# Kernel optimization log

Measured on AMD Instinct MI355X. Metric: run time of the kernel, lower is better.

Reference implementation:

```python
import jax, jax.numpy as jnp
import numpy as np
from jax import lax

DILATION_DEPTH = 10
N_REPEAT = 5
DILS = [2 ** i for i in range(DILATION_DEPTH)] * N_REPEAT  # 50 layers
N_RES, N_SKIP, N_FEAT = 32, 512, 8
B, T = 4, 16384


def _dconv(x, w, b, d):
    # valid (causal, no padding) dilated conv1d, kernel size 2: out[t] = w0*x[t] + w1*x[t+d]
    y = lax.conv_general_dilated(x, w, window_strides=(1,), padding='VALID',
                                 rhs_dilation=(d,), dimension_numbers=('NCH', 'OIH', 'NCH'))
    return y + b[None, :, None]


def _pw(x, w, b):
    # 1x1 conv as einsum; w: [out, in]
    return jnp.einsum('oc,bct->bot', w, x) + b[None, :, None]


def setup_inputs() -> dict:
    key = jax.random.key(0)
    ks = jax.random.split(key, 16)
    L = len(DILS)
    s = 0.1
    return {
        'input': jax.random.normal(ks[0], (B, T, N_FEAT), dtype=jnp.float32),
        'from_w': jax.random.normal(ks[1], (N_RES, N_FEAT, 1), dtype=jnp.float32) * s,
        'from_b': jax.random.normal(ks[2], (N_RES,), dtype=jnp.float32) * s,
        'sig_w': jax.random.normal(ks[3], (L, N_RES, N_RES, 2), dtype=jnp.float32) * s,
        'sig_b': jax.random.normal(ks[4], (L, N_RES), dtype=jnp.float32) * s,
        'tan_w': jax.random.normal(ks[5], (L, N_RES, N_RES, 2), dtype=jnp.float32) * s,
        'tan_b': jax.random.normal(ks[6], (L, N_RES), dtype=jnp.float32) * s,
        'skip_w': jax.random.normal(ks[7], (L, N_SKIP, N_RES, 1), dtype=jnp.float32) * s,
        'skip_b': jax.random.normal(ks[8], (L, N_SKIP), dtype=jnp.float32) * s,
        'res_w': jax.random.normal(ks[9], (L, N_RES, N_RES, 1), dtype=jnp.float32) * s,
        'res_b': jax.random.normal(ks[10], (L, N_RES), dtype=jnp.float32) * s,
        'post1_w': jax.random.normal(ks[11], (N_SKIP, N_SKIP, 1), dtype=jnp.float32) * s,
        'post1_b': jax.random.normal(ks[12], (N_SKIP,), dtype=jnp.float32) * s,
        'post2_w': jax.random.normal(ks[13], (1, N_SKIP, 1), dtype=jnp.float32) * s,
        'post2_b': jax.random.normal(ks[14], (1,), dtype=jnp.float32) * s,
    }


def reference(input, from_w, from_b, sig_w, sig_b, tan_w, tan_b,
              skip_w, skip_b, res_w, res_b, post1_w, post1_b, post2_w, post2_b):
    h = jnp.transpose(input, (0, 2, 1))                       # [B, F, T]
    h = _pw(h, from_w[:, :, 0], from_b)                       # [B, 32, T]
    Lout = h.shape[2] - sum(DILS)                             # final output length
    skip_sum = jnp.zeros((h.shape[0], N_SKIP, Lout), dtype=h.dtype)
    for i, d in enumerate(DILS):
        gate = jax.nn.sigmoid(_dconv(h, sig_w[i], sig_b[i], d)) * \
               jnp.tanh(_dconv(h, tan_w[i], tan_b[i], d))      # [B, 32, T_i - d]
        skip = _pw(gate, skip_w[i, :, :, 0], skip_b[i])        # [B, 512, T_i - d]
        skip_sum = skip_sum + skip[:, :, -Lout:]
        h = _pw(gate, res_w[i, :, :, 0], res_b[i]) + h[:, :, d:]
    o = jax.nn.elu(skip_sum)
    o = _pw(o, post1_w[:, :, 0], post1_b)
    o = jax.nn.elu(o)
    o = _pw(o, post2_w[:, :, 0], post2_b)                     # [B, 1, Lout]
    return o
```

## Files before the change

### kernel.cpp

```cpp
#include <hip/hip_runtime.h>
#include <hip/hip_bf16.h>

#define TLEN 16384
#define NB 4
#define NLAYER 50
#define SUMD 5115
#define LOUT 11269
#define K1 (NLAYER * 32)
#define MSKIP 512
#define FWOUT 256
#define FWIN 511
#define FP 36

typedef unsigned short u16;
typedef __attribute__((ext_vector_type(4))) float f32x4;
typedef __attribute__((ext_vector_type(8))) __bf16 bf16x8;

__device__ __forceinline__ u16 f2bf(float f) {
  __hip_bfloat16 h = __float2bfloat16(f);
  return *reinterpret_cast<u16*>(&h);
}
__device__ __forceinline__ float bf2f(u16 u) {
  __hip_bfloat16 h = *reinterpret_cast<__hip_bfloat16*>(&u);
  return __bfloat162float(h);
}

__global__ __launch_bounds__(256) void prep_k(
    const float* __restrict__ skip_w, const float* __restrict__ skip_b,
    const float* __restrict__ post1_w,
    const float* __restrict__ sig_w, const float* __restrict__ tan_w,
    const float* __restrict__ res_w,
    u16* __restrict__ Wskip, u16* __restrict__ P1, float* __restrict__ biasS,
    u16* __restrict__ WC, u16* __restrict__ RC) {
  int t = blockIdx.x * 256 + threadIdx.x;
  const int n1 = 512 * K1;
  const int n2 = n1 + 512 * 512;
  const int n3 = n2 + 512;
  const int n4 = n3 + NLAYER * 64 * 64;
  const int n5 = n4 + NLAYER * 32 * 32;
  if (t < n1) {
    int m = t / K1, k = t - m * K1;
    int i = k >> 5, c = k & 31;
    Wskip[t] = f2bf(skip_w[((size_t)i * 512 + m) * 32 + c]);
  } else if (t < n2) {
    int z = t - n1;
    P1[z] = f2bf(post1_w[z]);
  } else if (t < n3) {
    int c = t - n2;
    float s = 0.f;
    for (int i = 0; i < NLAYER; i++) s += skip_b[i * 512 + c];
    biasS[c] = s;
  } else if (t < n4) {
    int z = t - n3;
    int l = z >> 12, rem = z & 4095, o = rem >> 6, k = rem & 63;
    int c = k & 31, lr = k >> 5;
    float v;
    if (o < 32) v = sig_w[(((size_t)l * 32 + o) * 32 + c) * 2 + lr];
    else        v = tan_w[(((size_t)l * 32 + (o - 32)) * 32 + c) * 2 + lr];
    WC[z] = f2bf(v);
  } else if (t < n5) {
    int z = t - n4;
    int l = z >> 10, rem = z & 1023, o = rem >> 5, c = rem & 31;
    RC[z] = f2bf(res_w[((size_t)l * 32 + o) * 32 + c]);
  }
}

__global__ __launch_bounds__(256) void init_p(
    const float* __restrict__ inp, const float* __restrict__ fw,
    const float* __restrict__ fb, float* __restrict__ H, int t0, int cw) {
  __shared__ float FWs[256];
  __shared__ float FBs[32];
  int tid = threadIdx.x;
  FWs[tid] = fw[tid];
  if (tid < 32) FBs[tid] = fb[tid];
  __syncthreads();
  int gsz = gridDim.x * 256;
  int gid0 = blockIdx.x * 256 + tid;
  for (int b = 0; b < NB; b++) {
    const float* ib = inp + ((size_t)b * TLEN + t0) * 8;
    float* hb = H + (size_t)b * cw * 32;
    for (int p = gid0; p < cw; p += gsz) {
      float4 x0 = *reinterpret_cast<const float4*>(ib + (size_t)p * 8);
      float4 x1 = *reinterpret_cast<const float4*>(ib + (size_t)p * 8 + 4);
      float x[8] = {x0.x, x0.y, x0.z, x0.w, x1.x, x1.y, x1.z, x1.w};
      float* op = hb + (size_t)p * 32;
      #pragma unroll
      for (int r4 = 0; r4 < 8; r4++) {
        float4 o;
        #pragma unroll
        for (int j = 0; j < 4; j++) {
          int r = r4 * 4 + j;
          float acc = FBs[r];
          #pragma unroll
          for (int f = 0; f < 8; f++) acc += FWs[r * 8 + f] * x[f];
          ((float*)&o)[j] = acc;
        }
        *reinterpret_cast<float4*>(op + r4 * 4) = o;
      }
    }
  }
}

__global__ __launch_bounds__(512, 1) void fuse8_k(
    const float* __restrict__ src, float* __restrict__ dst,
    u16* __restrict__ G,
    const u16* __restrict__ WC, const u16* __restrict__ RC,
    const float* __restrict__ sb, const float* __restrict__ tb,
    const float* __restrict__ rb,
    int L0, int len_in, int cw, int clen) {
  __shared__ float HB[2][FWIN][FP];
  __shared__ u16 GT[8][16][40];
  int tid = threadIdx.x;
  int wv = tid >> 6, lane = tid & 63;
  int pc = lane & 15, kg = lane >> 4;
  int b = blockIdx.y;
  int len_out = len_in - 255;
  int pstart = cw - len_out + blockIdx.x * FWOUT;
  int g0 = pstart - 255;
  int wcount = (cw - g0 < FWIN) ? (cw - g0) : FWIN;
  int ocount = (cw - pstart < FWOUT) ? (cw - pstart) : FWOUT;

  const float* sp = src + ((size_t)b * cw + g0) * 32;
  for (int z = tid; z < wcount * 8; z += 512) {
    int lp = z >> 3, c4 = z & 7;
    *reinterpret_cast<float4*>(&HB[0][lp][c4 * 4]) =
        *reinterpret_cast<const float4*>(sp + (size_t)lp * 32 + c4 * 4);
  }
  __syncthreads();

  int cur = 0;
  for (int l = 0; l < 8; l++) {
    int d = 1 << l;
    int cumD = (2 << l) - 1;
    const u16* Wc = WC + (size_t)(L0 + l) * 4096;
    const u16* Rc = RC + (size_t)(L0 + l) * 1024;
    bf16x8 AW[4][2], AR[2];
    #pragma unroll
    for (int mt = 0; mt < 4; mt++) {
      AW[mt][0] = *reinterpret_cast<const bf16x8*>(Wc + (mt * 16 + pc) * 64 + kg * 8);
      AW[mt][1] = *reinterpret_cast<const bf16x8*>(Wc + (mt * 16 + pc) * 64 + 32 + kg * 8);
    }
    AR[0] = *reinterpret_cast<const bf16x8*>(Rc + pc * 32 + kg * 8);
    AR[1] = *reinterpret_cast<const bf16x8*>(Rc + (16 + pc) * 32 + kg * 8);
    float4 sbv0 = *reinterpret_cast<const float4*>(sb + (L0 + l) * 32 + kg * 4);
    float4 sbv1 = *reinterpret_cast<const float4*>(sb + (L0 + l) * 32 + 16 + kg * 4);
    float4 tbv0 = *reinterpret_cast<const float4*>(tb + (L0 + l) * 32 + kg * 4);
    float4 tbv1 = *reinterpret_cast<const float4*>(tb + (L0 + l) * 32 + 16 + kg * 4);
    float4 rbv0 = *reinterpret_cast<const float4*>(rb + (L0 + l) * 32 + kg * 4);
    float4 rbv1 = *reinterpret_cast<const float4*>(rb + (L0 + l) * 32 + 16 + kg * 4);

    int lo_local = wcount - cumD;
    int nit = (lo_local + 127) >> 7;
    for (int t = 0; t < nit; t++) {
      int lp = cumD + t * 128 + wv * 16 + pc;
      bool valid = lp < wcount;
      int lpc = valid ? lp : wcount - 1;

      float4 r0 = *reinterpret_cast<const float4*>(&HB[cur][lpc][kg * 8]);
      float4 r1 = *reinterpret_cast<const float4*>(&HB[cur][lpc][kg * 8 + 4]);
      float4 l0v = *reinterpret_cast<const float4*>(&HB[cur][lpc - d][kg * 8]);
      float4 l1v = *reinterpret_cast<const float4*>(&HB[cur][lpc - d][kg * 8 + 4]);

      union { u16 u[8]; bf16x8 v; } uL, uR;
      {
        float lf[8] = {l0v.x, l0v.y, l0v.z, l0v.w, l1v.x, l1v.y, l1v.z, l1v.w};
        float rf[8] = {r0.x, r0.y, r0.z, r0.w, r1.x, r1.y, r1.z, r1.w};
        #pragma unroll
        for (int j = 0; j < 8; j++) { uL.u[j] = f2bf(lf[j]); uR.u[j] = f2bf(rf[j]); }
      }

      f32x4 cs0 = {0.f, 0.f, 0.f, 0.f}, cs1 = {0.f, 0.f, 0.f, 0.f};
      f32x4 ct0 = {0.f, 0.f, 0.f, 0.f}, ct1 = {0.f, 0.f, 0.f, 0.f};
      cs0 = __builtin_amdgcn_mfma_f32_16x16x32_bf16(AW[0][0], uL.v, cs0, 0, 0, 0);
      cs0 = __builtin_amdgcn_mfma_f32_16x16x32_bf16(AW[0][1], uR.v, cs0, 0, 0, 0);
      cs1 = __builtin_amdgcn_mfma_f32_16x16x32_bf16(AW[1][0], uL.v, cs1, 0, 0, 0);
      cs1 = __builtin_amdgcn_mfma_f32_16x16x32_bf16(AW[1][1], uR.v, cs1, 0, 0, 0);
      ct0 = __builtin_amdgcn_mfma_f32_16x16x32_bf16(AW[2][0], uL.v, ct0, 0, 0, 0);
      ct0 = __builtin_amdgcn_mfma_f32_16x16x32_bf16(AW[2][1], uR.v, ct0, 0, 0, 0);
      ct1 = __builtin_amdgcn_mfma_f32_16x16x32_bf16(AW[3][0], uL.v, ct1, 0, 0, 0);
      ct1 = __builtin_amdgcn_mfma_f32_16x16x32_bf16(AW[3][1], uR.v, ct1, 0, 0, 0);

      u16 gs0[4], gs1[4];
      {
        float sa[4] = {sbv0.x, sbv0.y, sbv0.z, sbv0.w};
        float sbq[4] = {sbv1.x, sbv1.y, sbv1.z, sbv1.w};
        float ta[4] = {tbv0.x, tbv0.y, tbv0.z, tbv0.w};
        float tbq[4] = {tbv1.x, tbv1.y, tbv1.z, tbv1.w};
        #pragma unroll
        for (int r = 0; r < 4; r++) {
          float s0 = cs0[r] + sa[r], t0v = ct0[r] + ta[r];
          float s1 = cs1[r] + sbq[r], t1v = ct1[r] + tbq[r];
          float g0v = (1.f / (1.f + __expf(-s0))) * (2.f / (1.f + __expf(-2.f * t0v)) - 1.f);
          float g1v = (1.f / (1.f + __expf(-s1))) * (2.f / (1.f + __expf(-2.f * t1v)) - 1.f);
          gs0[r] = f2bf(g0v);
          gs1[r] = f2bf(g1v);
        }
      }
      uint2 pk0 = {(unsigned)gs0[0] | ((unsigned)gs0[1] << 16),
                   (unsigned)gs0[2] | ((unsigned)gs0[3] << 16)};
      uint2 pk1 = {(unsigned)gs1[0] | ((unsigned)gs1[1] << 16),
                   (unsigned)gs1[2] | ((unsigned)gs1[3] << 16)};
      *reinterpret_cast<uint2*>(&GT[wv][pc][kg * 4]) = pk0;
      *reinterpret_cast<uint2*>(&GT[wv][pc][16 + kg * 4]) = pk1;

      int p = g0 + lpc;
      if (valid && p >= pstart && p < pstart + ocount && p >= cw - clen) {
        int n = b * clen + (p - (cw - clen));
        u16* gr = G + (size_t)n * K1 + (L0 + l) * 32;
        *reinterpret_cast<uint2*>(gr + kg * 4) = pk0;
        *reinterpret_cast<uint2*>(gr + 16 + kg * 4) = pk1;
      }

      bf16x8 bg = *reinterpret_cast<const bf16x8*>(&GT[wv][pc][kg * 8]);
      float4 ha = *reinterpret_cast<const float4*>(&HB[cur][lpc][kg * 4]);
      float4 hb2 = *reinterpret_cast<const float4*>(&HB[cur][lpc][16 + kg * 4]);
      f32x4 h0 = {ha.x + rbv0.x, ha.y + rbv0.y, ha.z + rbv0.z, ha.w + rbv0.w};
      f32x4 h1 = {hb2.x + rbv1.x, hb2.y + rbv1.y, hb2.z + rbv1.z, hb2.w + rbv1.w};
      f32x4 d0 = __builtin_amdgcn_mfma_f32_16x16x32_bf16(AR[0], bg, h0, 0, 0, 0);
      f32x4 d1 = __builtin_amdgcn_mfma_f32_16x16x32_bf16(AR[1], bg, h1, 0, 0, 0);
      if (valid) {
        *reinterpret_cast<float4*>(&HB[cur ^ 1][lp][kg * 4]) = float4{d0[0], d0[1], d0[2], d0[3]};
        *reinterpret_cast<float4*>(&HB[cur ^ 1][lp][16 + kg * 4]) = float4{d1[0], d1[1], d1[2], d1[3]};
      }
    }
    __syncthreads();
    cur ^= 1;
  }

  float* dp = dst + ((size_t)b * cw + pstart) * 32;
  for (int z = tid; z < ocount * 8; z += 512) {
    int lp = z >> 3, c4 = z & 7;
    *reinterpret_cast<float4*>(dp + (size_t)lp * 32 + c4 * 4) =
        *reinterpret_cast<float4*>(&HB[cur][255 + lp][c4 * 4]);
  }
}

__global__ __launch_bounds__(256, 2) void layer_p(
    const float* __restrict__ src, float* __restrict__ dst,
    u16* __restrict__ G,
    const u16* __restrict__ Wc, const u16* __restrict__ Rc,
    const float* __restrict__ sbl, const float* __restrict__ tbl,
    const float* __restrict__ rbl,
    int layer, int d, int lo, int cw, int clen) {
  __shared__ u16 GT[4][16][40];
  __shared__ float HRT[4][16][36];
  int tid = threadIdx.x;
  int wv = tid >> 6, lane = tid & 63;
  int pc = lane & 15, kg = lane >> 4;
  int b = blockIdx.y;

  bf16x8 AW[4][2], AR[2];
  #pragma unroll
  for (int mt = 0; mt < 4; mt++) {
    AW[mt][0] = *reinterpret_cast<const bf16x8*>(Wc + (mt * 16 + pc) * 64 + kg * 8);
    AW[mt][1] = *reinterpret_cast<const bf16x8*>(Wc + (mt * 16 + pc) * 64 + 32 + kg * 8);
  }
  AR[0] = *reinterpret_cast<const bf16x8*>(Rc + pc * 32 + kg * 8);
  AR[1] = *reinterpret_cast<const bf16x8*>(Rc + (16 + pc) * 32 + kg * 8);

  float4 sbv0 = *reinterpret_cast<const float4*>(sbl + kg * 4);
  float4 sbv1 = *reinterpret_cast<const float4*>(sbl + 16 + kg * 4);
  float4 tbv0 = *reinterpret_cast<const float4*>(tbl + kg * 4);
  float4 tbv1 = *reinterpret_cast<const float4*>(tbl + 16 + kg * 4);
  float4 rbv0 = *reinterpret_cast<const float4*>(rbl + kg * 4);
  float4 rbv1 = *reinterpret_cast<const float4*>(rbl + 16 + kg * 4);

  int idx = blockIdx.x * 64 + wv * 16 + pc;
  bool valid = idx < lo;
  int idc = valid ? idx : lo - 1;
  int p = cw - lo + idc;

  const float* hp = src + ((size_t)b * cw + p) * 32 + kg * 8;
  float4 r0 = *reinterpret_cast<const float4*>(hp);
  float4 r1 = *reinterpret_cast<const float4*>(hp + 4);
  const float* hq = hp - (size_t)d * 32;
  float4 l0 = *reinterpret_cast<const float4*>(hq);
  float4 l1 = *reinterpret_cast<const float4*>(hq + 4);

  union { u16 u[8]; bf16x8 v; } uL, uR;
  {
    float lf[8] = {l0.x, l0.y, l0.z, l0.w, l1.x, l1.y, l1.z, l1.w};
    float rf[8] = {r0.x, r0.y, r0.z, r0.w, r1.x, r1.y, r1.z, r1.w};
    #pragma unroll
    for (int j = 0; j < 8; j++) { uL.u[j] = f2bf(lf[j]); uR.u[j] = f2bf(rf[j]); }
  }
  *reinterpret_cast<float4*>(&HRT[wv][pc][kg * 8]) = r0;
  *reinterpret_cast<float4*>(&HRT[wv][pc][kg * 8 + 4]) = r1;

  f32x4 cs0 = {0.f, 0.f, 0.f, 0.f}, cs1 = {0.f, 0.f, 0.f, 0.f};
  f32x4 ct0 = {0.f, 0.f, 0.f, 0.f}, ct1 = {0.f, 0.f, 0.f, 0.f};
  cs0 = __builtin_amdgcn_mfma_f32_16x16x32_bf16(AW[0][0], uL.v, cs0, 0, 0, 0);
  cs0 = __builtin_amdgcn_mfma_f32_16x16x32_bf16(AW[0][1], uR.v, cs0, 0, 0, 0);
  cs1 = __builtin_amdgcn_mfma_f32_16x16x32_bf16(AW[1][0], uL.v, cs1, 0, 0, 0);
  cs1 = __builtin_amdgcn_mfma_f32_16x16x32_bf16(AW[1][1], uR.v, cs1, 0, 0, 0);
  ct0 = __builtin_amdgcn_mfma_f32_16x16x32_bf16(AW[2][0], uL.v, ct0, 0, 0, 0);
  ct0 = __builtin_amdgcn_mfma_f32_16x16x32_bf16(AW[2][1], uR.v, ct0, 0, 0, 0);
  ct1 = __builtin_amdgcn_mfma_f32_16x16x32_bf16(AW[3][0], uL.v, ct1, 0, 0, 0);
  ct1 = __builtin_amdgcn_mfma_f32_16x16x32_bf16(AW[3][1], uR.v, ct1, 0, 0, 0);

  u16 gs0[4], gs1[4];
  {
    float sa[4] = {sbv0.x, sbv0.y, sbv0.z, sbv0.w};
    float sbq[4] = {sbv1.x, sbv1.y, sbv1.z, sbv1.w};
    float ta[4] = {tbv0.x, tbv0.y, tbv0.z, tbv0.w};
    float tbq[4] = {tbv1.x, tbv1.y, tbv1.z, tbv1.w};
    #pragma unroll
    for (int r = 0; r < 4; r++) {
      float s0 = cs0[r] + sa[r], t0v = ct0[r] + ta[r];
      float s1 = cs1[r] + sbq[r], t1v = ct1[r] + tbq[r];
      float g0 = (1.f / (1.f + __expf(-s0))) * (2.f / (1.f + __expf(-2.f * t0v)) - 1.f);
      float g1 = (1.f / (1.f + __expf(-s1))) * (2.f / (1.f + __expf(-2.f * t1v)) - 1.f);
      gs0[r] = f2bf(g0);
      gs1[r] = f2bf(g1);
    }
  }
  uint2 pk0 = {(unsigned)gs0[0] | ((unsigned)gs0[1] << 16),
               (unsigned)gs0[2] | ((unsigned)gs0[3] << 16)};
  uint2 pk1 = {(unsigned)gs1[0] | ((unsigned)gs1[1] << 16),
               (unsigned)gs1[2] | ((unsigned)gs1[3] << 16)};
  *reinterpret_cast<uint2*>(&GT[wv][pc][kg * 4]) = pk0;
  *reinterpret_cast<uint2*>(&GT[wv][pc][16 + kg * 4]) = pk1;

  if (valid && p >= cw - clen) {
    int n = b * clen + (p - (cw - clen));
    u16* gr = G + (size_t)n * K1 + layer * 32;
    *reinterpret_cast<uint2*>(gr + kg * 4) = pk0;
    *reinterpret_cast<uint2*>(gr + 16 + kg * 4) = pk1;
  }

  bf16x8 bg = *reinterpret_cast<const bf16x8*>(&GT[wv][pc][kg * 8]);
  float4 ha = *reinterpret_cast<const float4*>(&HRT[wv][pc][kg * 4]);
  float4 hbq = *reinterpret_cast<const float4*>(&HRT[wv][pc][16 + kg * 4]);
  f32x4 h0 = {ha.x + rbv0.x, ha.y + rbv0.y, ha.z + rbv0.z, ha.w + rbv0.w};
  f32x4 h1 = {hbq.x + rbv1.x, hbq.y + rbv1.y, hbq.z + rbv1.z, hbq.w + rbv1.w};
  f32x4 d0 = __builtin_amdgcn_mfma_f32_16x16x32_bf16(AR[0], bg, h0, 0, 0, 0);
  f32x4 d1 = __builtin_amdgcn_mfma_f32_16x16x32_bf16(AR[1], bg, h1, 0, 0, 0);
  if (valid) {
    float* dp = dst + ((size_t)b * cw + p) * 32;
    *reinterpret_cast<float4*>(dp + kg * 4) = float4{d0[0], d0[1], d0[2], d0[3]};
    *reinterpret_cast<float4*>(dp + 16 + kg * 4) = float4{d1[0], d1[1], d1[2], d1[3]};
  }
}

__global__ __launch_bounds__(256) void gemm_k(
    const u16* __restrict__ A, const u16* __restrict__ B,
    const float* __restrict__ bias, u16* __restrict__ Out,
    int N, int K) {
  __shared__ u16 As[128][72];
  __shared__ u16 Bs[128][72];
  int tid = threadIdx.x;

  int nwg = gridDim.x;
  int orig = blockIdx.x;
  int q = nwg >> 3, r8 = nwg & 7, xcd = orig & 7, sl = orig >> 3;
  int wg = (xcd < r8 ? xcd * (q + 1) : r8 * (q + 1) + (xcd - r8) * q) + sl;
  int m0 = (wg & 3) * 128;
  int n0 = (wg >> 2) * 128;

  int lane = tid & 63, w = tid >> 6;
  int wm = w >> 1, wn = w & 1;

  f32x4 acc[4][4];
  #pragma unroll
  for (int i = 0; i < 4; i++)
    #pragma unroll
    for (int j = 0; j < 4; j++) acc[i][j] = f32x4{0.f, 0.f, 0.f, 0.f};

  int rS = tid >> 1, qS = tid & 1;
  for (int k0 = 0; k0 < K; k0 += 64) {
    {
      const uint4* asrc = reinterpret_cast<const uint4*>(A + (size_t)(m0 + rS) * K + k0 + qS * 32);
      uint4 a0 = asrc[0], a1 = asrc[1], a2 = asrc[2], a3 = asrc[3];
      *reinterpret_cast<uint4*>(&As[rS][qS * 32]) = a0;
      *reinterpret_cast<uint4*>(&As[rS][qS * 32 + 8]) = a1;
      *reinterpret_cast<uint4*>(&As[rS][qS * 32 + 16]) = a2;
      *reinterpret_cast<uint4*>(&As[rS][qS * 32 + 24]) = a3;
    }
    {
      int nr = n0 + rS;
      uint4 b0 = {0,0,0,0}, b1 = {0,0,0,0}, b2 = {0,0,0,0}, b3 = {0,0,0,0};
      if (nr < N) {
        const uint4* bsrc = reinterpret_cast<const uint4*>(B + (size_t)nr * K + k0 + qS * 32);
        b0 = bsrc[0]; b1 = bsrc[1]; b2 = bsrc[2]; b3 = bsrc[3];
      }
      *reinterpret_cast<uint4*>(&Bs[rS][qS * 32]) = b0;
      *reinterpret_cast<uint4*>(&Bs[rS][qS * 32 + 8]) = b1;
      *reinterpret_cast<uint4*>(&Bs[rS][qS * 32 + 16]) = b2;
      *reinterpret_cast<uint4*>(&Bs[rS][qS * 32 + 24]) = b3;
    }
    __syncthreads();

    int row16 = lane & 15, kg = lane >> 4;
    #pragma unroll
    for (int s = 0; s < 2; s++) {
      bf16x8 af[4], bfr[4];
      #pragma unroll
      for (int mf = 0; mf < 4; mf++)
        af[mf] = *reinterpret_cast<const bf16x8*>(&As[wm * 64 + mf * 16 + row16][s * 32 + kg * 8]);
      #pragma unroll
      for (int nf = 0; nf < 4; nf++)
        bfr[nf] = *reinterpret_cast<const bf16x8*>(&Bs[wn * 64 + nf * 16 + row16][s * 32 + kg * 8]);
      #pragma unroll
      for (int mf = 0; mf < 4; mf++)
        #pragma unroll
        for (int nf = 0; nf < 4; nf++)
          acc[mf][nf] = __builtin_amdgcn_mfma_f32_16x16x32_bf16(af[mf], bfr[nf], acc[mf][nf], 0, 0, 0);
    }
    __syncthreads();
  }

  #pragma unroll
  for (int mf = 0; mf < 4; mf++) {
    int rowb = m0 + wm * 64 + mf * 16 + (lane >> 4) * 4;
    float b0 = bias[rowb], b1 = bias[rowb + 1], b2 = bias[rowb + 2], b3 = bias[rowb + 3];
    #pragma unroll
    for (int nf = 0; nf < 4; nf++) {
      int col = n0 + wn * 64 + nf * 16 + (lane & 15);
      if (col < N) {
        float v0 = acc[mf][nf][0] + b0, v1 = acc[mf][nf][1] + b1;
        float v2 = acc[mf][nf][2] + b2, v3 = acc[mf][nf][3] + b3;
        v0 = v0 > 0.f ? v0 : expm1f(v0);
        v1 = v1 > 0.f ? v1 : expm1f(v1);
        v2 = v2 > 0.f ? v2 : expm1f(v2);
        v3 = v3 > 0.f ? v3 : expm1f(v3);
        uint2 pk = {(unsigned)f2bf(v0) | ((unsigned)f2bf(v1) << 16),
                    (unsigned)f2bf(v2) | ((unsigned)f2bf(v3) << 16)};
        *reinterpret_cast<uint2*>(Out + (size_t)col * 512 + rowb) = pk;
      }
    }
  }
}

__global__ __launch_bounds__(256) void final_k(
    const u16* __restrict__ E2, const float* __restrict__ w,
    const float* __restrict__ bptr, float* __restrict__ out,
    int Nc, int clen, int t0) {
  int gid = blockIdx.x * 256 + threadIdx.x;
  int n = gid >> 2, qq = gid & 3;
  if (n >= Nc) return;
  const uint4* row = reinterpret_cast<const uint4*>(E2 + (size_t)n * 512 + qq * 128);
  const float4* wq = reinterpret_cast<const float4*>(w + qq * 128);
  float acc = 0.f;
  #pragma unroll 4
  for (int c8 = 0; c8 < 16; c8++) {
    uint4 v = row[c8];
    float4 w0 = wq[c8 * 2], w1 = wq[c8 * 2 + 1];
    acc += w0.x * bf2f(v.x & 0xffff) + w0.y * bf2f(v.x >> 16)
         + w0.z * bf2f(v.y & 0xffff) + w0.w * bf2f(v.y >> 16)
         + w1.x * bf2f(v.z & 0xffff) + w1.y * bf2f(v.z >> 16)
         + w1.z * bf2f(v.w & 0xffff) + w1.w * bf2f(v.w >> 16);
  }
  acc += __shfl_xor(acc, 1);
  acc += __shfl_xor(acc, 2);
  if (qq == 0) {
    int b = n / clen, tc = n - b * clen;
    out[(size_t)b * LOUT + t0 + tc] = acc + bptr[0];
  }
}

extern "C" void kernel_launch(void* const* d_in, const int* in_sizes, int n_in,
                              void* d_out, int out_size, void* d_ws, size_t ws_size,
                              hipStream_t stream) {
  const float* input   = (const float*)d_in[0];
  const float* from_w  = (const float*)d_in[1];
  const float* from_b  = (const float*)d_in[2];
  const float* sig_w   = (const float*)d_in[3];
  const float* sig_b   = (const float*)d_in[4];
  const float* tan_w   = (const float*)d_in[5];
  const float* tan_b   = (const float*)d_in[6];
  const float* skip_w  = (const float*)d_in[7];
  const float* skip_b  = (const float*)d_in[8];
  const float* res_w   = (const float*)d_in[9];
  const float* res_b   = (const float*)d_in[10];
  const float* post1_w = (const float*)d_in[11];
  const float* post1_b = (const float*)d_in[12];
  const float* post2_w = (const float*)d_in[13];
  const float* post2_b = (const float*)d_in[14];

  auto al = [](size_t x) { return (x + 255) & ~(size_t)255; };
  size_t oW  = 0;
  size_t oP1 = oW  + al((size_t)512 * K1 * 2);
  size_t oB  = oP1 + al((size_t)512 * 512 * 2);
  size_t oWC = oB  + al((size_t)512 * 4);
  size_t oRC = oWC + al((size_t)NLAYER * 64 * 64 * 2);
  size_t wend = oRC + al((size_t)NLAYER * 32 * 32 * 2);

  int NC = 32, CL = 0;
  size_t oH0 = wend, oH1 = wend, oG = wend, oE = wend;
  const int cand[6] = {1, 2, 4, 8, 16, 32};
  for (int ci = 0; ci < 6; ci++) {
    int nc = cand[ci];
    int cl = (LOUT + nc - 1) / nc;
    int cw = cl + SUMD;
    size_t hB = al((size_t)NB * 32 * cw * 4);
    size_t gB = al((size_t)NB * cl * K1 * 2);
    size_t eB = al((size_t)512 * NB * cl * 2);
    size_t need = wend + 2 * hB + gB + eB;
    if (need <= ws_size || nc == 32) {
      NC = nc; CL = cl;
      oH0 = wend; oH1 = oH0 + hB; oG = oH1 + hB; oE = oG + gB;
      break;
    }
  }

  char* ws = (char*)d_ws;
  u16*   Wskip = (u16*)(ws + oW);
  u16*   P1    = (u16*)(ws + oP1);
  float* biasS = (float*)(ws + oB);
  u16*   WC    = (u16*)(ws + oWC);
  u16*   RC    = (u16*)(ws + oRC);
  float* H0    = (float*)(ws + oH0);
  float* H1    = (float*)(ws + oH1);
  u16*   G     = (u16*)(ws + oG);
  u16*   E     = (u16*)(ws + oE);
  u16*   E2    = (u16*)(ws + oG);

  int prep_items = 512 * K1 + 512 * 512 + 512 + NLAYER * 64 * 64 + NLAYER * 32 * 32;
  prep_k<<<(prep_items + 255) / 256, 256, 0, stream>>>(
      skip_w, skip_b, post1_w, sig_w, tan_w, res_w, Wskip, P1, biasS, WC, RC);

  for (int c = 0; c < NC; c++) {
    int t0 = c * CL;
    if (t0 >= LOUT) break;
    int clen = LOUT - t0 < CL ? LOUT - t0 : CL;
    int cw = clen + SUMD;

    init_p<<<256, 256, 0, stream>>>(input, from_w, from_b, H0, t0, cw);

    float* a = H0;
    float* b2 = H1;
    int len = cw;
    for (int cyc = 0; cyc < 5; cyc++) {
      int L0 = cyc * 10;
      int lo8 = len - 255;
      int tiles = (lo8 + FWOUT - 1) / FWOUT;
      fuse8_k<<<dim3(tiles, NB), 512, 0, stream>>>(
          a, b2, G, WC, RC, sig_b, tan_b, res_b, L0, len, cw, clen);
      { float* t = a; a = b2; b2 = t; }
      len = lo8;
      {
        int li = L0 + 8, d = 256;
        int lo = len - d;
        layer_p<<<dim3((lo + 63) / 64, NB), 256, 0, stream>>>(
            a, b2, G, WC + (size_t)li * 4096, RC + (size_t)li * 1024,
            sig_b + li * 32, tan_b + li * 32, res_b + li * 32,
            li, d, lo, cw, clen);
        { float* t = a; a = b2; b2 = t; }
        len = lo;
      }
      {
        int li = L0 + 9, d = 512;
        int lo = len - d;
        layer_p<<<dim3((lo + 63) / 64, NB), 256, 0, stream>>>(
            a, b2, G, WC + (size_t)li * 4096, RC + (size_t)li * 1024,
            sig_b + li * 32, tan_b + li * 32, res_b + li * 32,
            li, d, lo, cw, clen);
        { float* t = a; a = b2; b2 = t; }
        len = lo;
      }
    }

    int Nc = NB * clen;
    int ntile = (Nc + 127) / 128;
    gemm_k<<<4 * ntile, 256, 0, stream>>>(Wskip, G, biasS, E, Nc, K1);
    gemm_k<<<4 * ntile, 256, 0, stream>>>(P1, E, post1_b, E2, Nc, 512);

    final_k<<<(4 * Nc + 255) / 256, 256, 0, stream>>>(E2, post2_w, post2_b, (float*)d_out, Nc, clen, t0);
  }
}
```

Measured before the change: 709.7 us.

## Fuse final projection into post1 GEMM epilogue and use direct global-to-LDS loads

The final 512-to-1 projection is folded into the post1 GEMM epilogue. Each tile reduces its partial dot products across lanes and atomically adds them into the output, which is zeroed beforehand with a memset. This removes the E2 intermediate write and read and one kernel launch per chunk. The GEMM main loop also switches to global_load_lds direct loads with K-step 32 and unpadded LDS, which can add LDS bank conflicts and more barrier iterations; the atomics make the summation order nondeterministic.

```diff
diff --git a/kernel.cpp b/kernel.cpp
--- a/kernel.cpp
+++ b/kernel.cpp
@@ -345,9 +345,11 @@
 __global__ __launch_bounds__(256) void gemm_k(
     const u16* __restrict__ A, const u16* __restrict__ B,
     const float* __restrict__ bias, u16* __restrict__ Out,
-    int N, int K) {
-  __shared__ u16 As[128][72];
-  __shared__ u16 Bs[128][72];
+    const float* __restrict__ w2, const float* __restrict__ b2p,
+    float* __restrict__ outv,
+    int N, int K, int FIN, int clen, int t0f) {
+  __shared__ __align__(16) u16 As[128 * 32];
+  __shared__ __align__(16) u16 Bs[128 * 32];
   int tid = threadIdx.x;
 
   int nwg = gridDim.x;
@@ -357,8 +359,10 @@
   int m0 = (wg & 3) * 128;
   int n0 = (wg >> 2) * 128;
 
-  int lane = tid & 63, w = tid >> 6;
-  int wm = w >> 1, wn = w & 1;
+  int lane = tid & 63, wv = tid >> 6;
+  int wm = wv >> 1, wn = wv & 1;
+  int row16 = lane & 15, kg = lane >> 4;
+  int l3 = lane & 3, lr = lane >> 2;
 
   f32x4 acc[4][4];
   #pragma unroll
@@ -366,95 +370,92 @@
     #pragma unroll
     for (int j = 0; j < 4; j++) acc[i][j] = f32x4{0.f, 0.f, 0.f, 0.f};
 
-  int rS = tid >> 1, qS = tid & 1;
-  for (int k0 = 0; k0 < K; k0 += 64) {
-    {
-      const uint4* asrc = reinterpret_cast<const uint4*>(A + (size_t)(m0 + rS) * K + k0 + qS * 32);
-      uint4 a0 = asrc[0], a1 = asrc[1], a2 = asrc[2], a3 = asrc[3];
-      *reinterpret_cast<uint4*>(&As[rS][qS * 32]) = a0;
-      *reinterpret_cast<uint4*>(&As[rS][qS * 32 + 8]) = a1;
-      *reinterpret_cast<uint4*>(&As[rS][qS * 32 + 16]) = a2;
-      *reinterpret_cast<uint4*>(&As[rS][qS * 32 + 24]) = a3;
-    }
-    {
-      int nr = n0 + rS;
-      uint4 b0 = {0,0,0,0}, b1 = {0,0,0,0}, b2 = {0,0,0,0}, b3 = {0,0,0,0};
-      if (nr < N) {
-        const uint4* bsrc = reinterpret_cast<const uint4*>(B + (size_t)nr * K + k0 + qS * 32);
-        b0 = bsrc[0]; b1 = bsrc[1]; b2 = bsrc[2]; b3 = bsrc[3];
-      }
-      *reinterpret_cast<uint4*>(&Bs[rS][qS * 32]) = b0;
-      *reinterpret_cast<uint4*>(&Bs[rS][qS * 32 + 8]) = b1;
-      *reinterpret_cast<uint4*>(&Bs[rS][qS * 32 + 16]) = b2;
-      *reinterpret_cast<uint4*>(&Bs[rS][qS * 32 + 24]) = b3;
+  for (int k0 = 0; k0 < K; k0 += 32) {
+    #pragma unroll
+    for (int i = 0; i < 2; i++) {
+      int c = wv * 2 + i;
+      int row = c * 16 + lr;
+      const u16* ga = A + (size_t)(m0 + row) * K + k0 + l3 * 8;
+      __builtin_amdgcn_global_load_lds(
+          (const __attribute__((address_space(1))) void*)ga,
+          (__attribute__((address_space(3))) void*)(As + c * 512), 16, 0, 0);
+      int nr = n0 + row;
+      if (nr > N - 1) nr = N - 1;
+      const u16* gb = B + (size_t)nr * K + k0 + l3 * 8;
+      __builtin_amdgcn_global_load_lds(
+          (const __attribute__((address_space(1))) void*)gb,
+          (__attribute__((address_space(3))) void*)(Bs + c * 512), 16, 0, 0);
     }
     __syncthreads();
 
-    int row16 = lane & 15, kg = lane >> 4;
-    #pragma unroll
-    for (int s = 0; s < 2; s++) {
-      bf16x8 af[4], bfr[4];
-      #pragma unroll
-      for (int mf = 0; mf < 4; mf++)
-        af[mf] = *reinterpret_cast<const bf16x8*>(&As[wm * 64 + mf * 16 + row16][s * 32 + kg * 8]);
+    bf16x8 af[4], bfr[4];
+    #pragma unroll
+    for (int mf = 0; mf < 4; mf++)
+      af[mf] = *reinterpret_cast<const bf16x8*>(&As[(wm * 64 + mf * 16 + row16) * 32 + kg * 8]);
+    #pragma unroll
+    for (int nf = 0; nf < 4; nf++)
+      bfr[nf] = *reinterpret_cast<const bf16x8*>(&Bs[(wn * 64 + nf * 16 + row16) * 32 + kg * 8]);
+    #pragma unroll
+    for (int mf = 0; mf < 4; mf++)
       #pragma unroll
       for (int nf = 0; nf < 4; nf++)
-        bfr[nf] = *reinterpret_cast<const bf16x8*>(&Bs[wn * 64 + nf * 16 + row16][s * 32 + kg * 8]);
+        acc[mf][nf] = __builtin_amdgcn_mfma_f32_16x16x32_bf16(af[mf], bfr[nf], acc[mf][nf], 0, 0, 0);
+    __syncthreads();
+  }
+
+  if (!FIN) {
+    #pragma unroll
+    for (int mf = 0; mf < 4; mf++) {
+      int rowb = m0 + wm * 64 + mf * 16 + kg * 4;
+      float b0 = bias[rowb], b1 = bias[rowb + 1], b2 = bias[rowb + 2], b3 = bias[rowb + 3];
       #pragma unroll
-      for (int mf = 0; mf < 4; mf++)
-        #pragma unroll
-        for (int nf = 0; nf < 4; nf++)
-          acc[mf][nf] = __builtin_amdgcn_mfma_f32_16x16x32_bf16(af[mf], bfr[nf], acc[mf][nf], 0, 0, 0);
-    }
-    __syncthreads();
-  }
-
-  #pragma unroll
-  for (int mf = 0; mf < 4; mf++) {
-    int rowb = m0 + wm * 64 + mf * 16 + (lane >> 4) * 4;
-    float b0 = bias[rowb], b1 = bias[rowb + 1], b2 = bias[rowb + 2], b3 = bias[rowb + 3];
-    #pragma unroll
-    for (int nf = 0; nf < 4; nf++) {
-      int col = n0 + wn * 64 + nf * 16 + (lane & 15);
-      if (col < N) {
+      for (int nf = 0; nf < 4; nf++) {
+        int col = n0 + wn * 64 + nf * 16 + row16;
+        if (col < N) {
+          float v0 = acc[mf][nf][0] + b0, v1 = acc[mf][nf][1] + b1;
+          float v2 = acc[mf][nf][2] + b2, v3 = acc[mf][nf][3] + b3;
+          v0 = v0 > 0.f ? v0 : expm1f(v0);
+          v1 = v1 > 0.f ? v1 : expm1f(v1);
+          v2 = v2 > 0.f ? v2 : expm1f(v2);
+          v3 = v3 > 0.f ? v3 : expm1f(v3);
+          uint2 pk = {(unsigned)f2bf(v0) | ((unsigned)f2bf(v1) << 16),
+                      (unsigned)f2bf(v2) | ((unsigned)f2bf(v3) << 16)};
+          *reinterpret_cast<uint2*>(Out + (size_t)col * 512 + rowb) = pk;
+        }
+      }
+    }
+  } else {
+    float part[4] = {0.f, 0.f, 0.f, 0.f};
+    #pragma unroll
+    for (int mf = 0; mf < 4; mf++) {
+      int rowb = m0 + wm * 64 + mf * 16 + kg * 4;
+      float b0 = bias[rowb], b1 = bias[rowb + 1], b2 = bias[rowb + 2], b3 = bias[rowb + 3];
+      float w0 = w2[rowb], w1 = w2[rowb + 1], w2v = w2[rowb + 2], w3 = w2[rowb + 3];
+      #pragma unroll
+      for (int nf = 0; nf < 4; nf++) {
         float v0 = acc[mf][nf][0] + b0, v1 = acc[mf][nf][1] + b1;
         float v2 = acc[mf][nf][2] + b2, v3 = acc[mf][nf][3] + b3;
         v0 = v0 > 0.f ? v0 : expm1f(v0);
         v1 = v1 > 0.f ? v1 : expm1f(v1);
         v2 = v2 > 0.f ? v2 : expm1f(v2);
         v3 = v3 > 0.f ? v3 : expm1f(v3);
-        uint2 pk = {(unsigned)f2bf(v0) | ((unsigned)f2bf(v1) << 16),
-                    (unsigned)f2bf(v2) | ((unsigned)f2bf(v3) << 16)};
-        *reinterpret_cast<uint2*>(Out + (size_t)col * 512 + rowb) = pk;
-      }
-    }
-  }
-}
-
-__global__ __launch_bounds__(256) void final_k(
-    const u16* __restrict__ E2, const float* __restrict__ w,
-    const float* __restrict__ bptr, float* __restrict__ out,
-    int Nc, int clen, int t0) {
-  int gid = blockIdx.x * 256 + threadIdx.x;
-  int n = gid >> 2, qq = gid & 3;
-  if (n >= Nc) return;
-  const uint4* row = reinterpret_cast<const uint4*>(E2 + (size_t)n * 512 + qq * 128);
-  const float4* wq = reinterpret_cast<const float4*>(w + qq * 128);
-  float acc = 0.f;
-  #pragma unroll 4
-  for (int c8 = 0; c8 < 16; c8++) {
-    uint4 v = row[c8];
-    float4 w0 = wq[c8 * 2], w1 = wq[c8 * 2 + 1];
-    acc += w0.x * bf2f(v.x & 0xffff) + w0.y * bf2f(v.x >> 16)
-         + w0.z * bf2f(v.y & 0xffff) + w0.w * bf2f(v.y >> 16)
-         + w1.x * bf2f(v.z & 0xffff) + w1.y * bf2f(v.z >> 16)
-         + w1.z * bf2f(v.w & 0xffff) + w1.w * bf2f(v.w >> 16);
-  }
-  acc += __shfl_xor(acc, 1);
-  acc += __shfl_xor(acc, 2);
-  if (qq == 0) {
-    int b = n / clen, tc = n - b * clen;
-    out[(size_t)b * LOUT + t0 + tc] = acc + bptr[0];
+        part[nf] += w0 * v0 + w1 * v1 + w2v * v2 + w3 * v3;
+      }
+    }
+    #pragma unroll
+    for (int nf = 0; nf < 4; nf++) {
+      float p = part[nf];
+      p += __shfl_xor(p, 16);
+      p += __shfl_xor(p, 32);
+      if (kg == 0) {
+        int col = n0 + wn * 64 + nf * 16 + row16;
+        if (col < N) {
+          if (m0 == 0 && wm == 0) p += b2p[0];
+          int bb = col / clen, tc = col - bb * clen;
+          atomicAdd(outv + (size_t)bb * LOUT + t0f + tc, p);
+        }
+      }
+    }
   }
 }
 
@@ -513,7 +514,8 @@
   float* H1    = (float*)(ws + oH1);
   u16*   G     = (u16*)(ws + oG);
   u16*   E     = (u16*)(ws + oE);
-  u16*   E2    = (u16*)(ws + oG);
+
+  hipMemsetAsync(d_out, 0, (size_t)out_size * sizeof(float), stream);
 
   int prep_items = 512 * K1 + 512 * 512 + 512 + NLAYER * 64 * 64 + NLAYER * 32 * 32;
   prep_k<<<(prep_items + 255) / 256, 256, 0, stream>>>(
@@ -538,8 +540,8 @@
           a, b2, G, WC, RC, sig_b, tan_b, res_b, L0, len, cw, clen);
       { float* t = a; a = b2; b2 = t; }
       len = lo8;
-      {
-        int li = L0 + 8, d = 256;
+      for (int j = 0; j < 2; j++) {
+        int li = L0 + 8 + j, d = 256 << j;
         int lo = len - d;
         layer_p<<<dim3((lo + 63) / 64, NB), 256, 0, stream>>>(
             a, b2, G, WC + (size_t)li * 4096, RC + (size_t)li * 1024,
@@ -548,23 +550,15 @@
         { float* t = a; a = b2; b2 = t; }
         len = lo;
       }
-      {
-        int li = L0 + 9, d = 512;
-        int lo = len - d;
-        layer_p<<<dim3((lo + 63) / 64, NB), 256, 0, stream>>>(
-            a, b2, G, WC + (size_t)li * 4096, RC + (size_t)li * 1024,
-            sig_b + li * 32, tan_b + li * 32, res_b + li * 32,
-            li, d, lo, cw, clen);
-        { float* t = a; a = b2; b2 = t; }
-        len = lo;
-      }
     }
 
     int Nc = NB * clen;
     int ntile = (Nc + 127) / 128;
-    gemm_k<<<4 * ntile, 256, 0, stream>>>(Wskip, G, biasS, E, Nc, K1);
-    gemm_k<<<4 * ntile, 256, 0, stream>>>(P1, E, post1_b, E2, Nc, 512);
-
-    final_k<<<(4 * Nc + 255) / 256, 256, 0, stream>>>(E2, post2_w, post2_b, (float*)d_out, Nc, clen, t0);
-  }
-}
+    gemm_k<<<4 * ntile, 256, 0, stream>>>(Wskip, G, biasS, E,
+                                          post2_w, post2_b, (float*)d_out,
+                                          Nc, K1, 0, clen, t0);
+    gemm_k<<<4 * ntile, 256, 0, stream>>>(P1, E, post1_b, E,
+                                          post2_w, post2_b, (float*)d_out,
+                                          Nc, 512, 1, clen, t0);
+  }
+}
```

After: 728.7 us. +2.7%, slower.
